# Optimization experiments

Measured on AMD Instinct MI355X. Metric: run time of the kernel, lower is better.

Reference implementation:

```python
import jax, jax.numpy as jnp
import numpy as np

UP = jnp.array([0.0, 1.0, 0.0], dtype=jnp.float32)
LEASH = 15.0


def q_inv(q):
    return jnp.concatenate([-q[..., :3], q[..., 3:]], axis=-1)


def q_mul(q1, q2):
    x1, y1, z1, w1 = q1[..., 0], q1[..., 1], q1[..., 2], q1[..., 3]
    x2, y2, z2, w2 = q2[..., 0], q2[..., 1], q2[..., 2], q2[..., 3]
    return jnp.stack([
        w1 * x2 + x1 * w2 + y1 * z2 - z1 * y2,
        w1 * y2 - x1 * z2 + y1 * w2 + z1 * x2,
        w1 * z2 + x1 * y2 - y1 * x2 + z1 * w2,
        w1 * w2 - x1 * x2 - y1 * y2 - z1 * z2], axis=-1)


def q_rot(q, v):
    qv, qw = q[..., :3], q[..., 3:]
    t = 2.0 * jnp.cross(qv, v)
    return v + qw * t + jnp.cross(qv, t)


def mat_to_quat(R):
    # Batched [E,3,3] -> [E,4] (x,y,z,w), matching the torch branch structure.
    r = lambda i, j: R[:, i, j]
    eps = 1e-12
    tr = r(0, 0) + r(1, 1) + r(2, 2)
    Sa = jnp.sqrt(jnp.maximum(tr + 1.0, eps)) * 2.0
    qa = jnp.stack([(r(2, 1) - r(1, 2)) / Sa, (r(0, 2) - r(2, 0)) / Sa,
                    (r(1, 0) - r(0, 1)) / Sa, 0.25 * Sa], -1)
    Sb = jnp.sqrt(jnp.maximum(1.0 + r(0, 0) - r(1, 1) - r(2, 2), eps)) * 2.0
    qb = jnp.stack([0.25 * Sb, (r(0, 1) + r(1, 0)) / Sb,
                    (r(0, 2) + r(2, 0)) / Sb, (r(2, 1) - r(1, 2)) / Sb], -1)
    Sc = jnp.sqrt(jnp.maximum(1.0 + r(1, 1) - r(0, 0) - r(2, 2), eps)) * 2.0
    qc = jnp.stack([(r(0, 1) + r(1, 0)) / Sc, 0.25 * Sc,
                    (r(1, 2) + r(2, 1)) / Sc, (r(0, 2) - r(2, 0)) / Sc], -1)
    Sd = jnp.sqrt(jnp.maximum(1.0 + r(2, 2) - r(0, 0) - r(1, 1), eps)) * 2.0
    qd = jnp.stack([(r(0, 2) + r(2, 0)) / Sd, (r(1, 2) + r(2, 1)) / Sd,
                    0.25 * Sd, (r(1, 0) - r(0, 1)) / Sd], -1)
    cond_b = ((r(0, 0) > r(1, 1)) & (r(0, 0) > r(2, 2)))[:, None]
    cond_c = (r(1, 1) > r(2, 2))[:, None]
    return jnp.where((tr > 0)[:, None], qa,
                     jnp.where(cond_b, qb, jnp.where(cond_c, qc, qd)))


def sfm_pose_loss(pred_t, pred_q, gt_t, gt_q, batch_counts):
    E = batch_counts.shape[0]
    N = pred_t.shape[0]
    counts = batch_counts.astype(jnp.float32)  # [E]
    seg = jnp.repeat(jnp.arange(E), batch_counts, total_repeat_length=N)  # [N]
    starts = jnp.cumsum(batch_counts) - batch_counts  # first index of each episode
    sseg = lambda x: jax.ops.segment_sum(x, seg, num_segments=E)

    # --- per-episode centering ---
    mu_p = sseg(pred_t) / counts[:, None]
    mu_g = sseg(gt_t) / counts[:, None]
    p_c = pred_t - mu_p[seg]
    g_c = gt_t - mu_g[seg]

    # degenerate episodes: too short or near-zero gt variance (unbiased var)
    g_var = sseg(jnp.sum(g_c ** 2, -1)) / (counts - 1.0)
    deg = (batch_counts < 4) | (g_var < 1e-4)  # [E]

    # --- Umeyama: batched 3x3 SVD of H = p_c^T @ g_c per episode ---
    H = sseg(p_c[:, :, None] * g_c[:, None, :])  # [E,3,3]
    H_safe = jnp.where(deg[:, None, None], jnp.diag(jnp.array([3.0, 2.0, 1.0])), H)
    U, S, Vh = jnp.linalg.svd(H_safe, full_matrices=False)
    V = jnp.swapaxes(Vh, -1, -2)
    R0 = jnp.einsum('eij,ekj->eik', V, U)  # V @ U^T
    sgn = jnp.where(jnp.linalg.det(R0) < 0, -1.0, 1.0)
    V_adj = V * jnp.stack([jnp.ones_like(sgn), jnp.ones_like(sgn), sgn], -1)[:, None, :]
    R = jnp.einsum('eij,ekj->eik', V_adj, U)  # [E,3,3]

    p_rot = jnp.einsum('nij,nj->ni', R[seg], p_c)
    denom = sseg(jnp.sum(p_c ** 2, -1))
    nom = sseg(jnp.sum(p_rot * g_c, -1))
    s = jnp.where(denom > 1e-6,
                  jnp.clip(nom / jnp.maximum(denom, 1e-6), 1e-3, 1e3), 1.0)

    # --- translation loss (per-episode mse, then mean over episodes) ---
    p_al = jnp.where(deg[seg][:, None], p_c, p_rot * s[seg][:, None])
    diff = p_al - g_c
    loss_trans = jnp.mean(sseg(jnp.sum(diff ** 2, -1)) / (counts * 3.0))

    # --- scale loss (only non-degenerate episodes) ---
    loss_scale = jnp.sum(jnp.where(deg, 0.0, jnp.log(jnp.abs(s) + 1e-6) ** 2)) / E

    # --- rotation loss ---
    q_align = mat_to_quat(R)  # [E,4]
    q0_p = pred_q[starts]
    q0_g = gt_q[starts]
    pq_deg = q_mul(q_inv(q0_p)[seg], pred_q)
    gq_deg = q_mul(q_inv(q0_g)[seg], gt_q)
    pq_ume = q_mul(q_align[seg], pred_q)
    dm = deg[seg][:, None]
    pq_al = jnp.where(dm, pq_deg, pq_ume)
    gq_al = jnp.where(dm, gq_deg, gt_q)
    dot = jnp.sum(pq_al * gq_al, -1)
    loss_rot = jnp.mean(sseg(1.0 - dot ** 2) / counts)

    # --- gravity loss ---
    up = jnp.broadcast_to(UP, pred_q.shape[:-1] + (3,))
    pu = q_rot(q_inv(pred_q), up)
    gu = q_rot(q_inv(gt_q), up)
    cos = jnp.sum(pu * gu, -1) / jnp.maximum(
        jnp.linalg.norm(pu, axis=-1) * jnp.linalg.norm(gu, axis=-1), 1e-8)
    loss_grav = jnp.mean(sseg(1.0 - cos) / counts)

    # --- frame0 leash (deadzone on first translation of each episode) ---
    mag = jnp.linalg.norm(pred_t[starts], axis=-1)
    loss_leash = jnp.mean(jnp.maximum(mag - LEASH, 0.0) ** 2)

    return jnp.stack([loss_trans, loss_rot, loss_grav, loss_leash, loss_scale])


def setup_inputs() -> dict:
    rng = np.random.default_rng(0)
    E = 4096
    counts = rng.integers(64, 449, size=E)
    counts[:8] = np.array([2, 3, 3, 2, 3, 2, 3, 3])  # exercise degenerate branch
    N = int(counts.sum())
    key = jax.random.key(0)
    k1, k2, k3, k4 = jax.random.split(key, 4)
    pred_t = jax.random.normal(k1, (N, 3), dtype=jnp.float32) * 5.0
    gt_t = jax.random.normal(k2, (N, 3), dtype=jnp.float32) * 5.0

    def rand_unit_quat(k):
        q = jax.random.normal(k, (N, 4), dtype=jnp.float32)
        return q / jnp.linalg.norm(q, axis=-1, keepdims=True)

    return {
        'pred_t': pred_t,
        'pred_q': rand_unit_quat(k3),
        'gt_t': gt_t,
        'gt_q': rand_unit_quat(k4),
        'batch_counts': jnp.asarray(counts, dtype=jnp.int32),
    }


def reference(pred_t, pred_q, gt_t, gt_q, batch_counts):
    # Returns [loss_trans, loss_rot, loss_grav, loss_leash, loss_scale]
    return sfm_pose_loss(pred_t, pred_q, gt_t, gt_q, batch_counts)
```

## Files before the change

kernel.cpp:

```cpp
#include <hip/hip_runtime.h>
#include <math.h>

__global__ void scan_kernel(const int* __restrict__ counts,
                            int* __restrict__ starts,
                            float* __restrict__ out, int E) {
    __shared__ int lds[1024];
    int tid = threadIdx.x;
    if (tid < 5) out[tid] = 0.0f;
    int base = tid * 4;
    int c0 = (base + 0 < E) ? counts[base + 0] : 0;
    int c1 = (base + 1 < E) ? counts[base + 1] : 0;
    int c2 = (base + 2 < E) ? counts[base + 2] : 0;
    int c3 = (base + 3 < E) ? counts[base + 3] : 0;
    lds[tid] = c0 + c1 + c2 + c3;
    __syncthreads();
    for (int off = 1; off < 1024; off <<= 1) {
        int v = lds[tid];
        int a = (tid >= off) ? lds[tid - off] : 0;
        __syncthreads();
        lds[tid] = v + a;
        __syncthreads();
    }
    int excl = (tid > 0) ? lds[tid - 1] : 0;
    if (base + 0 < E) starts[base + 0] = excl; excl += c0;
    if (base + 1 < E) starts[base + 1] = excl; excl += c1;
    if (base + 2 < E) starts[base + 2] = excl; excl += c2;
    if (base + 3 < E) starts[base + 3] = excl;
}

__device__ __forceinline__ float4 qmul4(float4 a, float4 b) {
    return make_float4(
        a.w*b.x + a.x*b.w + a.y*b.z - a.z*b.y,
        a.w*b.y - a.x*b.z + a.y*b.w + a.z*b.x,
        a.w*b.z + a.x*b.y - a.y*b.x + a.z*b.w,
        a.w*b.w - a.x*b.x - a.y*b.y - a.z*b.z);
}

__device__ __forceinline__ void qinv_rot_up(float4 q, float out[3]) {
    float qx = -q.x, qy = -q.y, qz = -q.z, qw = q.w;
    float tx = -2.f*qz;
    float ty = 0.f;
    float tz = 2.f*qx;
    out[0] = 0.f + qw*tx + (qy*tz - qz*ty);
    out[1] = 1.f + qw*ty + (qz*tx - qx*tz);
    out[2] = 0.f + qw*tz + (qx*ty - qy*tx);
}

__device__ __forceinline__ float wave_sum(float v) {
    v += __shfl_xor(v, 32);
    v += __shfl_xor(v, 16);
    v += __shfl_xor(v, 8);
    v += __shfl_xor(v, 4);
    v += __shfl_xor(v, 2);
    v += __shfl_xor(v, 1);
    return v;
}

#define NS 29
__global__ __launch_bounds__(256) void pass1_kernel(
    const float* __restrict__ pred_t, const float4* __restrict__ pred_q,
    const float* __restrict__ gt_t,   const float4* __restrict__ gt_q,
    const int* __restrict__ counts, const int* __restrict__ starts,
    float* __restrict__ segacc, int E)
{
    int wv = threadIdx.x >> 6;
    int lane = threadIdx.x & 63;
    int e = blockIdx.x * 4 + wv;
    if (e >= E) return;
    int start = starts[e];
    int ci = counts[e];
    bool small_c = (ci < 4);
    float4 q0p = pred_q[start];
    float4 q0g = gt_q[start];
    float4 q0pi = make_float4(-q0p.x, -q0p.y, -q0p.z, q0p.w);
    float4 q0gi = make_float4(-q0g.x, -q0g.y, -q0g.z, q0g.w);

    float acc[NS];
    #pragma unroll
    for (int k = 0; k < NS; ++k) acc[k] = 0.f;

    int iters = (ci + 63) >> 6;
    int i = lane;
    int m = start + min(i, ci - 1);
    float px = pred_t[3*m+0], py = pred_t[3*m+1], pz = pred_t[3*m+2];
    float gx = gt_t[3*m+0],  gy = gt_t[3*m+1],  gz = gt_t[3*m+2];
    float4 pq = pred_q[m];
    float4 gq = gt_q[m];

    for (int j = 0; ; ) {
        float npx = 0.f, npy = 0.f, npz = 0.f, ngx = 0.f, ngy = 0.f, ngz = 0.f;
        float4 npq = make_float4(0.f,0.f,0.f,0.f), ngq = npq;
        bool have_next = (j + 1 < iters);
        if (have_next) {
            int m2 = start + min(i + 64, ci - 1);
            npx = pred_t[3*m2+0]; npy = pred_t[3*m2+1]; npz = pred_t[3*m2+2];
            ngx = gt_t[3*m2+0];  ngy = gt_t[3*m2+1];  ngz = gt_t[3*m2+2];
            npq = pred_q[m2];
            ngq = gt_q[m2];
        }
        if (i < ci) {
            acc[0] += px; acc[1] += py; acc[2] += pz;
            acc[3] += gx; acc[4] += gy; acc[5] += gz;
            acc[6] += px*px + py*py + pz*pz;
            acc[7] += gx*gx + gy*gy + gz*gz;
            acc[8]  += px*gx; acc[9]  += px*gy; acc[10] += px*gz;
            acc[11] += py*gx; acc[12] += py*gy; acc[13] += py*gz;
            acc[14] += pz*gx; acc[15] += pz*gy; acc[16] += pz*gz;

            float mx =  pq.w*gq.x - pq.z*gq.y + pq.y*gq.z - pq.x*gq.w;
            float my =  pq.z*gq.x + pq.w*gq.y - pq.x*gq.z - pq.y*gq.w;
            float mz = -pq.y*gq.x + pq.x*gq.y + pq.w*gq.z - pq.z*gq.w;
            float mw =  pq.x*gq.x + pq.y*gq.y + pq.z*gq.z + pq.w*gq.w;
            acc[17] += mx*mx; acc[18] += mx*my; acc[19] += mx*mz; acc[20] += mx*mw;
            acc[21] += my*my; acc[22] += my*mz; acc[23] += my*mw;
            acc[24] += mz*mz; acc[25] += mz*mw; acc[26] += mw*mw;

            float pu[3], gu[3];
            qinv_rot_up(pq, pu);
            qinv_rot_up(gq, gu);
            float cosv = pu[0]*gu[0] + pu[1]*gu[1] + pu[2]*gu[2];
            acc[27] += 1.f - cosv;

            if (small_c) {
                float4 aa = qmul4(q0pi, pq);
                float4 bb = qmul4(q0gi, gq);
                float dd = aa.x*bb.x + aa.y*bb.y + aa.z*bb.z + aa.w*bb.w;
                acc[28] += 1.f - dd*dd;
            }
        }
        if (!have_next) break;
        px = npx; py = npy; pz = npz;
        gx = ngx; gy = ngy; gz = ngz;
        pq = npq; gq = ngq;
        i += 64; ++j;
    }

    #pragma unroll
    for (int k = 0; k < NS; ++k) acc[k] = wave_sum(acc[k]);

    float outv = 0.f;
    #pragma unroll
    for (int k = 0; k < NS; ++k)
        if (lane == k) outv = acc[k];
    if (lane < NS)
        segacc[(size_t)e*32 + lane] = outv;
}

__device__ void jacobi3f(float A[3][3], float V[3][3]) {
    V[0][0]=1.f; V[0][1]=0.f; V[0][2]=0.f;
    V[1][0]=0.f; V[1][1]=1.f; V[1][2]=0.f;
    V[2][0]=0.f; V[2][1]=0.f; V[2][2]=1.f;
    for (int sweep = 0; sweep < 6; ++sweep) {
        float off = A[0][1]*A[0][1] + A[0][2]*A[0][2] + A[1][2]*A[1][2];
        float dia = A[0][0]*A[0][0] + A[1][1]*A[1][1] + A[2][2]*A[2][2];
        if (off <= 1e-12f * (dia + 1e-30f)) break;
        for (int p = 0; p < 2; ++p) for (int q = p + 1; q < 3; ++q) {
            float apq = A[p][q];
            if (fabsf(apq) < 1e-30f) continue;
            float theta = (A[q][q] - A[p][p]) / (2.0f * apq);
            float t = ((theta >= 0.f) ? 1.f : -1.f) / (fabsf(theta) + sqrtf(theta*theta + 1.f));
            float cc = 1.f / sqrtf(t*t + 1.f);
            float ss = t * cc;
            float app = A[p][p], aqq = A[q][q];
            A[p][p] = app - t * apq;
            A[q][q] = aqq + t * apq;
            A[p][q] = 0.f; A[q][p] = 0.f;
            int r = 3 - p - q;
            float arp = A[r][p], arq = A[r][q];
            A[r][p] = cc*arp - ss*arq; A[p][r] = A[r][p];
            A[r][q] = ss*arp + cc*arq; A[q][r] = A[r][q];
            for (int i = 0; i < 3; ++i) {
                float vip = V[i][p], viq = V[i][q];
                V[i][p] = cc*vip - ss*viq;
                V[i][q] = ss*vip + cc*viq;
            }
        }
    }
}

__device__ void mat2quatf(const float R[3][3], float q[4]) {
    const float eps = 1e-12f;
    float tr = R[0][0] + R[1][1] + R[2][2];
    if (tr > 0.f) {
        float S = sqrtf(fmaxf(tr + 1.f, eps)) * 2.f;
        q[0] = (R[2][1]-R[1][2])/S; q[1] = (R[0][2]-R[2][0])/S;
        q[2] = (R[1][0]-R[0][1])/S; q[3] = 0.25f*S;
    } else if ((R[0][0] > R[1][1]) && (R[0][0] > R[2][2])) {
        float S = sqrtf(fmaxf(1.f + R[0][0] - R[1][1] - R[2][2], eps)) * 2.f;
        q[0] = 0.25f*S; q[1] = (R[0][1]+R[1][0])/S;
        q[2] = (R[0][2]+R[2][0])/S; q[3] = (R[2][1]-R[1][2])/S;
    } else if (R[1][1] > R[2][2]) {
        float S = sqrtf(fmaxf(1.f + R[1][1] - R[0][0] - R[2][2], eps)) * 2.f;
        q[0] = (R[0][1]+R[1][0])/S; q[1] = 0.25f*S;
        q[2] = (R[1][2]+R[2][1])/S; q[3] = (R[0][2]-R[2][0])/S;
    } else {
        float S = sqrtf(fmaxf(1.f + R[2][2] - R[0][0] - R[1][1], eps)) * 2.f;
        q[0] = (R[0][2]+R[2][0])/S; q[1] = (R[1][2]+R[2][1])/S;
        q[2] = 0.25f*S; q[3] = (R[1][0]-R[0][1])/S;
    }
}

__global__ __launch_bounds__(64) void finalize_kernel(
    const float* __restrict__ segacc, const int* __restrict__ counts,
    const int* __restrict__ starts, const float* __restrict__ pred_t,
    const float4* __restrict__ pred_q, const float4* __restrict__ gt_q,
    float* __restrict__ out, int E)
{
    int e = blockIdx.x * 64 + threadIdx.x;
    float v_trans = 0.f, v_rot = 0.f, v_grav = 0.f, v_leash = 0.f, v_scale = 0.f;
    if (e < E) {
        const float* A = segacc + (size_t)e * 32;
        int ci = counts[e];
        int start = starts[e];
        float c = (float)ci;
        float mu_p[3] = { A[0]/c, A[1]/c, A[2]/c };
        float mu_g[3] = { A[3]/c, A[4]/c, A[5]/c };
        float pp_c = A[6] - c*(mu_p[0]*mu_p[0]+mu_p[1]*mu_p[1]+mu_p[2]*mu_p[2]);
        float gg_c = A[7] - c*(mu_g[0]*mu_g[0]+mu_g[1]*mu_g[1]+mu_g[2]*mu_g[2]);
        float H[3][3];
        H[0][0]=A[8] -c*mu_p[0]*mu_g[0]; H[0][1]=A[9] -c*mu_p[0]*mu_g[1]; H[0][2]=A[10]-c*mu_p[0]*mu_g[2];
        H[1][0]=A[11]-c*mu_p[1]*mu_g[0]; H[1][1]=A[12]-c*mu_p[1]*mu_g[1]; H[1][2]=A[13]-c*mu_p[1]*mu_g[2];
        H[2][0]=A[14]-c*mu_p[2]*mu_g[0]; H[2][1]=A[15]-c*mu_p[2]*mu_g[1]; H[2][2]=A[16]-c*mu_p[2]*mu_g[2];
        float g_var = gg_c / (c - 1.0f);
        bool small_c = (ci < 4);
        bool deg = small_c || (g_var < 1e-4f);
        float trans, rot, scale = 0.f;
        if (deg) {
            float s28;
            if (small_c) {
                s28 = A[28];
            } else {
                float4 q0p = pred_q[start];
                float4 q0g = gt_q[start];
                float4 q0pi = make_float4(-q0p.x, -q0p.y, -q0p.z, q0p.w);
                float4 q0gi = make_float4(-q0g.x, -q0g.y, -q0g.z, q0g.w);
                float local = 0.f;
                for (int ii = 0; ii < ci; ++ii) {
                    float4 aa = qmul4(q0pi, pred_q[start + ii]);
                    float4 bb = qmul4(q0gi, gt_q[start + ii]);
                    float dd = aa.x*bb.x + aa.y*bb.y + aa.z*bb.z + aa.w*bb.w;
                    local += 1.f - dd*dd;
                }
                s28 = local;
            }
            float trH = H[0][0] + H[1][1] + H[2][2];
            trans = (pp_c - 2.f*trH + gg_c) / (c * 3.f);
            rot = s28 / c;
        } else {
            float B[3][3], V[3][3];
            for (int i = 0; i < 3; ++i)
                for (int j = 0; j < 3; ++j)
                    B[i][j] = H[0][i]*H[0][j] + H[1][i]*H[1][j] + H[2][i]*H[2][j];
            jacobi3f(B, V);
            float lam[3] = { B[0][0], B[1][1], B[2][2] };
            int idx[3] = {0, 1, 2};
            if (lam[idx[0]] < lam[idx[1]]) { int t = idx[0]; idx[0] = idx[1]; idx[1] = t; }
            if (lam[idx[0]] < lam[idx[2]]) { int t = idx[0]; idx[0] = idx[2]; idx[2] = t; }
            if (lam[idx[1]] < lam[idx[2]]) { int t = idx[1]; idx[1] = idx[2]; idx[2] = t; }
            float v1[3], v2[3], v3[3];
            for (int i = 0; i < 3; ++i) { v1[i] = V[i][idx[0]]; v2[i] = V[i][idx[1]]; v3[i] = V[i][idx[2]]; }
            float detV = v1[0]*(v2[1]*v3[2]-v2[2]*v3[1])
                       - v1[1]*(v2[0]*v3[2]-v2[2]*v3[0])
                       + v1[2]*(v2[0]*v3[1]-v2[1]*v3[0]);
            float sgnV = (detV < 0.f) ? -1.f : 1.f;
            float u1[3], u2[3], u3[3];
            for (int i = 0; i < 3; ++i) u1[i] = H[i][0]*v1[0] + H[i][1]*v1[1] + H[i][2]*v1[2];
            float n1 = fmaxf(sqrtf(u1[0]*u1[0]+u1[1]*u1[1]+u1[2]*u1[2]), 1e-30f);
            for (int i = 0; i < 3; ++i) u1[i] /= n1;
            for (int i = 0; i < 3; ++i) u2[i] = H[i][0]*v2[0] + H[i][1]*v2[1] + H[i][2]*v2[2];
            float d12 = u1[0]*u2[0]+u1[1]*u2[1]+u1[2]*u2[2];
            for (int i = 0; i < 3; ++i) u2[i] -= d12*u1[i];
            float n2 = fmaxf(sqrtf(u2[0]*u2[0]+u2[1]*u2[1]+u2[2]*u2[2]), 1e-30f);
            for (int i = 0; i < 3; ++i) u2[i] /= n2;
            u3[0] = u1[1]*u2[2] - u1[2]*u2[1];
            u3[1] = u1[2]*u2[0] - u1[0]*u2[2];
            u3[2] = u1[0]*u2[1] - u1[1]*u2[0];
            float R[3][3];
            for (int i = 0; i < 3; ++i)
                for (int k = 0; k < 3; ++k)
                    R[i][k] = v1[i]*u1[k] + v2[i]*u2[k] + sgnV*v3[i]*u3[k];
            float nom = 0.f;
            for (int k = 0; k < 3; ++k)
                for (int j = 0; j < 3; ++j)
                    nom += R[k][j] * H[j][k];
            float denom = pp_c;
            float s = 1.f;
            if (denom > 1e-6f) {
                s = nom / fmaxf(denom, 1e-6f);
                s = fminf(fmaxf(s, 1e-3f), 1e3f);
            }
            trans = (s*s*denom - 2.f*s*nom + gg_c) / (c * 3.f);
            float ls = logf(fabsf(s) + 1e-6f);
            scale = ls * ls;
            float q[4];
            mat2quatf(R, q);
            float quad = q[0]*q[0]*A[17] + q[1]*q[1]*A[21] + q[2]*q[2]*A[24] + q[3]*q[3]*A[26]
                + 2.f*(q[0]*q[1]*A[18] + q[0]*q[2]*A[19] + q[0]*q[3]*A[20]
                     + q[1]*q[2]*A[22] + q[1]*q[3]*A[23] + q[2]*q[3]*A[25]);
            rot = (c - quad) / c;
        }
        float grav = A[27] / c;
        float tx = pred_t[3*start+0], ty = pred_t[3*start+1], tz = pred_t[3*start+2];
        float mag = sqrtf(tx*tx + ty*ty + tz*tz);
        float ml = fmaxf(mag - 15.f, 0.f);
        float Ed = (float)E;
        v_trans = trans / Ed;
        v_rot   = rot / Ed;
        v_grav  = grav / Ed;
        v_leash = (ml * ml) / Ed;
        v_scale = scale / Ed;
    }
    float vals[5] = { v_trans, v_rot, v_grav, v_leash, v_scale };
    #pragma unroll
    for (int k = 0; k < 5; ++k) {
        float v = wave_sum(vals[k]);
        if (threadIdx.x == 0) atomicAdd(out + k, v);
    }
}

extern "C" void kernel_launch(void* const* d_in, const int* in_sizes, int n_in,
                              void* d_out, int out_size, void* d_ws, size_t ws_size,
                              hipStream_t stream) {
    const float*  pred_t = (const float*)d_in[0];
    const float4* pred_q = (const float4*)d_in[1];
    const float*  gt_t   = (const float*)d_in[2];
    const float4* gt_q   = (const float4*)d_in[3];
    const int*    counts = (const int*)d_in[4];
    int E = in_sizes[4];

    int* starts = (int*)d_ws;
    size_t off = ((size_t)E * sizeof(int) + 255) & ~(size_t)255;
    float* segacc = (float*)((char*)d_ws + off);

    scan_kernel<<<1, 1024, 0, stream>>>(counts, starts, (float*)d_out, E);
    pass1_kernel<<<(E + 3) / 4, 256, 0, stream>>>(pred_t, pred_q, gt_t, gt_q,
                                                  counts, starts, segacc, E);
    finalize_kernel<<<(E + 63) / 64, 64, 0, stream>>>(segacc, counts, starts, pred_t,
                                                      pred_q, gt_q, (float*)d_out, E);
}
```

Before: 118.5 us.

## Split episodes into 64-point chunks, one wave per chunk, reduce partials in finalize

The scan kernel now also builds per-episode chunk offsets and a chunk-to-episode map so pass1 assigns one wave to each 64-element chunk instead of one wave per whole episode. This balances work across waves and raises parallelism for variable episode lengths of up to 448 points. Finalize then sums the per-chunk partial rows for each episode. The cost is more partial writes and reads, a serial map-writing loop in the single-block scan, and a larger pass1 grid where many trailing waves exit early.

```diff
diff --git a/kernel.cpp b/kernel.cpp
--- a/kernel.cpp
+++ b/kernel.cpp
@@ -1,18 +1,25 @@
 #include <hip/hip_runtime.h>
 #include <math.h>
 
+#define NS 29
+
 __global__ void scan_kernel(const int* __restrict__ counts,
                             int* __restrict__ starts,
+                            int* __restrict__ chunkoff,
+                            int* __restrict__ map,
+                            int* __restrict__ tot,
                             float* __restrict__ out, int E) {
     __shared__ int lds[1024];
     int tid = threadIdx.x;
     if (tid < 5) out[tid] = 0.0f;
     int base = tid * 4;
-    int c0 = (base + 0 < E) ? counts[base + 0] : 0;
-    int c1 = (base + 1 < E) ? counts[base + 1] : 0;
-    int c2 = (base + 2 < E) ? counts[base + 2] : 0;
-    int c3 = (base + 3 < E) ? counts[base + 3] : 0;
-    lds[tid] = c0 + c1 + c2 + c3;
+    int c[4], nch[4];
+    #pragma unroll
+    for (int j = 0; j < 4; ++j) {
+        c[j] = (base + j < E) ? counts[base + j] : 0;
+        nch[j] = (c[j] + 63) >> 6;
+    }
+    lds[tid] = c[0] + c[1] + c[2] + c[3];
     __syncthreads();
     for (int off = 1; off < 1024; off <<= 1) {
         int v = lds[tid];
@@ -22,10 +29,36 @@
         __syncthreads();
     }
     int excl = (tid > 0) ? lds[tid - 1] : 0;
-    if (base + 0 < E) starts[base + 0] = excl; excl += c0;
-    if (base + 1 < E) starts[base + 1] = excl; excl += c1;
-    if (base + 2 < E) starts[base + 2] = excl; excl += c2;
-    if (base + 3 < E) starts[base + 3] = excl;
+    #pragma unroll
+    for (int j = 0; j < 4; ++j) {
+        if (base + j < E) starts[base + j] = excl;
+        excl += c[j];
+    }
+    __syncthreads();
+    lds[tid] = nch[0] + nch[1] + nch[2] + nch[3];
+    __syncthreads();
+    for (int off = 1; off < 1024; off <<= 1) {
+        int v = lds[tid];
+        int a = (tid >= off) ? lds[tid - off] : 0;
+        __syncthreads();
+        lds[tid] = v + a;
+        __syncthreads();
+    }
+    int coff = (tid > 0) ? lds[tid - 1] : 0;
+    #pragma unroll
+    for (int j = 0; j < 4; ++j) {
+        int e = base + j;
+        if (e < E) {
+            chunkoff[e] = coff;
+            for (int jj = 0; jj < nch[j]; ++jj)
+                map[coff + jj] = (e << 5) | jj;
+            coff += nch[j];
+        }
+    }
+    if (tid == 1023) {
+        chunkoff[E] = lds[1023];
+        tot[0] = lds[1023];
+    }
 }
 
 __device__ __forceinline__ float4 qmul4(float4 a, float4 b) {
@@ -56,83 +89,66 @@
     return v;
 }
 
-#define NS 29
 __global__ __launch_bounds__(256) void pass1_kernel(
     const float* __restrict__ pred_t, const float4* __restrict__ pred_q,
     const float* __restrict__ gt_t,   const float4* __restrict__ gt_q,
     const int* __restrict__ counts, const int* __restrict__ starts,
-    float* __restrict__ segacc, int E)
+    const int* __restrict__ map, const int* __restrict__ tot,
+    float* __restrict__ partial)
 {
-    int wv = threadIdx.x >> 6;
     int lane = threadIdx.x & 63;
-    int e = blockIdx.x * 4 + wv;
-    if (e >= E) return;
+    int gw = blockIdx.x * 4 + (threadIdx.x >> 6);
+    if (gw >= tot[0]) return;
+    int mv = map[gw];
+    int e = mv >> 5, j = mv & 31;
     int start = starts[e];
     int ci = counts[e];
-    bool small_c = (ci < 4);
-    float4 q0p = pred_q[start];
-    float4 q0g = gt_q[start];
-    float4 q0pi = make_float4(-q0p.x, -q0p.y, -q0p.z, q0p.w);
-    float4 q0gi = make_float4(-q0g.x, -q0g.y, -q0g.z, q0g.w);
+    int i = (j << 6) + lane;
+    bool valid = i < ci;
+    int n = start + (valid ? i : (ci - 1));
+
+    float px = pred_t[3*n+0], py = pred_t[3*n+1], pz = pred_t[3*n+2];
+    float gx = gt_t[3*n+0],  gy = gt_t[3*n+1],  gz = gt_t[3*n+2];
+    float4 pq = pred_q[n];
+    float4 gq = gt_q[n];
 
     float acc[NS];
     #pragma unroll
     for (int k = 0; k < NS; ++k) acc[k] = 0.f;
 
-    int iters = (ci + 63) >> 6;
-    int i = lane;
-    int m = start + min(i, ci - 1);
-    float px = pred_t[3*m+0], py = pred_t[3*m+1], pz = pred_t[3*m+2];
-    float gx = gt_t[3*m+0],  gy = gt_t[3*m+1],  gz = gt_t[3*m+2];
-    float4 pq = pred_q[m];
-    float4 gq = gt_q[m];
-
-    for (int j = 0; ; ) {
-        float npx = 0.f, npy = 0.f, npz = 0.f, ngx = 0.f, ngy = 0.f, ngz = 0.f;
-        float4 npq = make_float4(0.f,0.f,0.f,0.f), ngq = npq;
-        bool have_next = (j + 1 < iters);
-        if (have_next) {
-            int m2 = start + min(i + 64, ci - 1);
-            npx = pred_t[3*m2+0]; npy = pred_t[3*m2+1]; npz = pred_t[3*m2+2];
-            ngx = gt_t[3*m2+0];  ngy = gt_t[3*m2+1];  ngz = gt_t[3*m2+2];
-            npq = pred_q[m2];
-            ngq = gt_q[m2];
-        }
-        if (i < ci) {
-            acc[0] += px; acc[1] += py; acc[2] += pz;
-            acc[3] += gx; acc[4] += gy; acc[5] += gz;
-            acc[6] += px*px + py*py + pz*pz;
-            acc[7] += gx*gx + gy*gy + gz*gz;
-            acc[8]  += px*gx; acc[9]  += px*gy; acc[10] += px*gz;
-            acc[11] += py*gx; acc[12] += py*gy; acc[13] += py*gz;
-            acc[14] += pz*gx; acc[15] += pz*gy; acc[16] += pz*gz;
-
-            float mx =  pq.w*gq.x - pq.z*gq.y + pq.y*gq.z - pq.x*gq.w;
-            float my =  pq.z*gq.x + pq.w*gq.y - pq.x*gq.z - pq.y*gq.w;
-            float mz = -pq.y*gq.x + pq.x*gq.y + pq.w*gq.z - pq.z*gq.w;
-            float mw =  pq.x*gq.x + pq.y*gq.y + pq.z*gq.z + pq.w*gq.w;
-            acc[17] += mx*mx; acc[18] += mx*my; acc[19] += mx*mz; acc[20] += mx*mw;
-            acc[21] += my*my; acc[22] += my*mz; acc[23] += my*mw;
-            acc[24] += mz*mz; acc[25] += mz*mw; acc[26] += mw*mw;
-
-            float pu[3], gu[3];
-            qinv_rot_up(pq, pu);
-            qinv_rot_up(gq, gu);
-            float cosv = pu[0]*gu[0] + pu[1]*gu[1] + pu[2]*gu[2];
-            acc[27] += 1.f - cosv;
-
-            if (small_c) {
-                float4 aa = qmul4(q0pi, pq);
-                float4 bb = qmul4(q0gi, gq);
-                float dd = aa.x*bb.x + aa.y*bb.y + aa.z*bb.z + aa.w*bb.w;
-                acc[28] += 1.f - dd*dd;
-            }
-        }
-        if (!have_next) break;
-        px = npx; py = npy; pz = npz;
-        gx = ngx; gy = ngy; gz = ngz;
-        pq = npq; gq = ngq;
-        i += 64; ++j;
+    if (valid) {
+        acc[0] = px; acc[1] = py; acc[2] = pz;
+        acc[3] = gx; acc[4] = gy; acc[5] = gz;
+        acc[6] = px*px + py*py + pz*pz;
+        acc[7] = gx*gx + gy*gy + gz*gz;
+        acc[8]  = px*gx; acc[9]  = px*gy; acc[10] = px*gz;
+        acc[11] = py*gx; acc[12] = py*gy; acc[13] = py*gz;
+        acc[14] = pz*gx; acc[15] = pz*gy; acc[16] = pz*gz;
+
+        float mx =  pq.w*gq.x - pq.z*gq.y + pq.y*gq.z - pq.x*gq.w;
+        float my =  pq.z*gq.x + pq.w*gq.y - pq.x*gq.z - pq.y*gq.w;
+        float mz = -pq.y*gq.x + pq.x*gq.y + pq.w*gq.z - pq.z*gq.w;
+        float mw =  pq.x*gq.x + pq.y*gq.y + pq.z*gq.z + pq.w*gq.w;
+        acc[17] = mx*mx; acc[18] = mx*my; acc[19] = mx*mz; acc[20] = mx*mw;
+        acc[21] = my*my; acc[22] = my*mz; acc[23] = my*mw;
+        acc[24] = mz*mz; acc[25] = mz*mw; acc[26] = mw*mw;
+
+        float pu[3], gu[3];
+        qinv_rot_up(pq, pu);
+        qinv_rot_up(gq, gu);
+        acc[27] = 1.f - (pu[0]*gu[0] + pu[1]*gu[1] + pu[2]*gu[2]);
+    }
+    if (ci < 4) {
+        float4 q0p = pred_q[start];
+        float4 q0g = gt_q[start];
+        float4 q0pi = make_float4(-q0p.x, -q0p.y, -q0p.z, q0p.w);
+        float4 q0gi = make_float4(-q0g.x, -q0g.y, -q0g.z, q0g.w);
+        if (valid) {
+            float4 aa = qmul4(q0pi, pq);
+            float4 bb = qmul4(q0gi, gq);
+            float dd = aa.x*bb.x + aa.y*bb.y + aa.z*bb.z + aa.w*bb.w;
+            acc[28] = 1.f - dd*dd;
+        }
     }
 
     #pragma unroll
@@ -143,7 +159,7 @@
     for (int k = 0; k < NS; ++k)
         if (lane == k) outv = acc[k];
     if (lane < NS)
-        segacc[(size_t)e*32 + lane] = outv;
+        partial[(size_t)gw * 32 + lane] = outv;
 }
 
 __device__ void jacobi3f(float A[3][3], float V[3][3]) {
@@ -201,15 +217,24 @@
 }
 
 __global__ __launch_bounds__(64) void finalize_kernel(
-    const float* __restrict__ segacc, const int* __restrict__ counts,
-    const int* __restrict__ starts, const float* __restrict__ pred_t,
-    const float4* __restrict__ pred_q, const float4* __restrict__ gt_q,
-    float* __restrict__ out, int E)
+    const float* __restrict__ partial, const int* __restrict__ chunkoff,
+    const int* __restrict__ counts, const int* __restrict__ starts,
+    const float* __restrict__ pred_t, const float4* __restrict__ pred_q,
+    const float4* __restrict__ gt_q, float* __restrict__ out, int E)
 {
     int e = blockIdx.x * 64 + threadIdx.x;
     float v_trans = 0.f, v_rot = 0.f, v_grav = 0.f, v_leash = 0.f, v_scale = 0.f;
     if (e < E) {
-        const float* A = segacc + (size_t)e * 32;
+        int off = chunkoff[e];
+        int nch = chunkoff[e + 1] - off;
+        float A[NS];
+        #pragma unroll
+        for (int k = 0; k < NS; ++k) A[k] = 0.f;
+        for (int r = 0; r < nch; ++r) {
+            const float* row = partial + (size_t)(off + r) * 32;
+            #pragma unroll
+            for (int k = 0; k < NS; ++k) A[k] += row[k];
+        }
         int ci = counts[e];
         int start = starts[e];
         float c = (float)ci;
@@ -327,14 +352,22 @@
     const float4* gt_q   = (const float4*)d_in[3];
     const int*    counts = (const int*)d_in[4];
     int E = in_sizes[4];
-
-    int* starts = (int*)d_ws;
-    size_t off = ((size_t)E * sizeof(int) + 255) & ~(size_t)255;
-    float* segacc = (float*)((char*)d_ws + off);
-
-    scan_kernel<<<1, 1024, 0, stream>>>(counts, starts, (float*)d_out, E);
-    pass1_kernel<<<(E + 3) / 4, 256, 0, stream>>>(pred_t, pred_q, gt_t, gt_q,
-                                                  counts, starts, segacc, E);
-    finalize_kernel<<<(E + 63) / 64, 64, 0, stream>>>(segacc, counts, starts, pred_t,
-                                                      pred_q, gt_q, (float*)d_out, E);
-}
+    int N = in_sizes[0] / 3;
+    int maxchunks = N / 64 + E + 1;
+
+    auto align256 = [](size_t x) { return (x + 255) & ~(size_t)255; };
+    char* p = (char*)d_ws;
+    int* starts   = (int*)p;                 p += align256((size_t)E * 4);
+    int* chunkoff = (int*)p;                 p += align256((size_t)(E + 1) * 4);
+    int* tot      = (int*)p;                 p += 256;
+    int* map      = (int*)p;                 p += align256((size_t)maxchunks * 4);
+    float* partial = (float*)p;
+
+    scan_kernel<<<1, 1024, 0, stream>>>(counts, starts, chunkoff, map, tot,
+                                        (float*)d_out, E);
+    pass1_kernel<<<(maxchunks + 3) / 4, 256, 0, stream>>>(
+        pred_t, pred_q, gt_t, gt_q, counts, starts, map, tot, partial);
+    finalize_kernel<<<(E + 63) / 64, 64, 0, stream>>>(
+        partial, chunkoff, counts, starts, pred_t, pred_q, gt_q,
+        (float*)d_out, E);
+}
```

Result: slower. 148.0 us (+24.9%).
